# Performance work log

Measured on AMD Instinct MI355X. Metric: run time of the kernel, lower is better.

## Reference

```python
import jax, jax.numpy as jnp
import numpy as np
from jax import lax

T_LEN, BATCH, D_IN, D_HID, N_LAYERS = 512, 32, 512, 512, 4


def setup_inputs() -> dict:
    key = jax.random.key(0)
    kx, kw, ku = jax.random.split(key, 3)
    x = jax.random.normal(kx, (T_LEN, BATCH, D_IN), dtype=jnp.float32)
    # xavier-ish scale on input kernels to keep the relu recurrence stable
    W = jax.random.normal(kw, (N_LAYERS, D_HID, D_IN), dtype=jnp.float32) * (1.0 / np.sqrt(D_IN))
    b = jnp.zeros((N_LAYERS, D_HID), dtype=jnp.float32)
    # diagonal recurrent weights in [0,1) so |u|<=1 (non-exploding)
    u = jax.random.uniform(ku, (N_LAYERS, D_HID), dtype=jnp.float32)
    return {"x": x, "W": W, "b": b, "u": u}


def _indrnn_layer(x, W_l, b_l, u_l):
    # x: [T, B, Din]; precompute input projection as one big GEMM
    xh = jnp.einsum('tbd,hd->tbh', x, W_l) + b_l  # [T, B, Dh]
    h0 = jnp.zeros((x.shape[1], W_l.shape[0]), dtype=x.dtype)

    def step(h, xh_t):
        h_new = jax.nn.relu(xh_t + u_l * h)
        return h_new, h_new

    _, outs = lax.scan(step, h0, xh)
    return outs  # [T, B, Dh]


def reference(x, W, b, u):
    out = x
    for l in range(W.shape[0]):  # fixed small layer count
        out = _indrnn_layer(out, W[l], b[l], u[l])
    return out
```

## Files before the change

### kernel.cpp

```cpp
#include <hip/hip_runtime.h>
#include <hip/hip_bf16.h>

typedef short bf16x8 __attribute__((ext_vector_type(8)));
typedef float f32x4 __attribute__((ext_vector_type(4)));

#define T_LEN 512
#define BATCH 32
#define D 512
#define M_TOT (T_LEN * BATCH)
#define NLAYER 4

#define BM 128
#define BN 128
#define BK 64
#define NT (D / BK)
#define EP 72

#define CH 64
#define NCH (T_LEN / CH)

__global__ __launch_bounds__(256) void convert_k(const float* __restrict__ W,
                                                 const float* __restrict__ x,
                                                 __hip_bfloat16* __restrict__ Wb,
                                                 __hip_bfloat16* __restrict__ xb) {
    const int nW = NLAYER * D * D;
    const int nX = M_TOT * D;
    int i = (blockIdx.x * 256 + threadIdx.x) * 4;
    const float* src;
    __hip_bfloat16* dst;
    if (i < nW) {
        src = W + i;
        dst = Wb + i;
    } else {
        int k = i - nW;
        if (k >= nX) return;
        src = x + k;
        dst = xb + k;
    }
    float4 v = *(const float4*)src;
    __hip_bfloat16 h0 = __float2bfloat16(v.x);
    __hip_bfloat16 h1 = __float2bfloat16(v.y);
    __hip_bfloat16 h2 = __float2bfloat16(v.z);
    __hip_bfloat16 h3 = __float2bfloat16(v.w);
    ushort4 o;
    o.x = *(const unsigned short*)&h0;
    o.y = *(const unsigned short*)&h1;
    o.z = *(const unsigned short*)&h2;
    o.w = *(const unsigned short*)&h3;
    *(ushort4*)dst = o;
}

__global__ __launch_bounds__(256) void gemm_bt(const __hip_bfloat16* __restrict__ A,
                                               const __hip_bfloat16* __restrict__ Bt,
                                               const float* __restrict__ bias,
                                               __hip_bfloat16* __restrict__ Cb) {
    constexpr int K = D;
    constexpr int N = D;
    __shared__ __hip_bfloat16 smem[4 * BM * BK];
    __hip_bfloat16* const AsP[2] = {smem, smem + BM * BK};
    __hip_bfloat16* const BsP[2] = {smem + 2 * BM * BK, smem + 3 * BM * BK};

    const int tid  = threadIdx.x;
    const int wave = tid >> 6;
    const int lane = tid & 63;

    const int bid = blockIdx.x;
    const int xcd = bid & 7;
    const int j   = bid >> 3;
    const int bm  = xcd * 16 + (j >> 2);
    const int bn  = j & 3;

    const int wm = (wave >> 1) * 64;
    const int wn = (wave & 1) * 64;

    const int srow = lane >> 3;
    const int scol = ((lane & 7) ^ srow) * 8;

    const __hip_bfloat16* Ag = A  + (size_t)(bm * BM) * K;
    const __hip_bfloat16* Bg = Bt + (size_t)(bn * BN) * K;

    f32x4 acc[4][4] = {};

#define STAGE(buf, k0)                                                                               \
    do {                                                                                             \
        _Pragma("unroll") for (int jj = 0; jj < 4; ++jj) {                                           \
            const int rbase = (jj * 4 + wave) * 8;                                                   \
            __builtin_amdgcn_global_load_lds(                                                        \
                (const __attribute__((address_space(1))) void*)(Ag + (size_t)(rbase + srow) * K + (k0) + scol), \
                (__attribute__((address_space(3))) void*)(&AsP[buf][rbase * BK]), 16, 0, 0);         \
            __builtin_amdgcn_global_load_lds(                                                        \
                (const __attribute__((address_space(1))) void*)(Bg + (size_t)(rbase + srow) * K + (k0) + scol), \
                (__attribute__((address_space(3))) void*)(&BsP[buf][rbase * BK]), 16, 0, 0);         \
        }                                                                                            \
    } while (0)

#define COMPUTE(buf)                                                                                 \
    do {                                                                                             \
        bf16x8 af[4][2], bv[4][2];                                                                   \
        const int fr = lane & 15;                                                                    \
        const int kq = lane >> 4;                                                          \
        _Pragma("unroll") for (int mi = 0; mi < 4; ++mi) {                                           \
            const int r = wm + mi * 16 + fr;                                                         \
            _Pragma("unroll") for (int kh = 0; kh < 2; ++kh) {                                       \
                const int c = ((kh * 4 + kq) ^ (fr & 7)) * 8;                                        \
                af[mi][kh] = *(const bf16x8*)(&AsP[buf][r * BK + c]);                                \
            }                                                                                        \
        }                                                                                            \
        _Pragma("unroll") for (int ni = 0; ni < 4; ++ni) {                                           \
            const int r = wn + ni * 16 + fr;                                                         \
            _Pragma("unroll") for (int kh = 0; kh < 2; ++kh) {                                       \
                const int c = ((kh * 4 + kq) ^ (fr & 7)) * 8;                                        \
                bv[ni][kh] = *(const bf16x8*)(&BsP[buf][r * BK + c]);                                \
            }                                                                                        \
        }                                                                                            \
        _Pragma("unroll") for (int kh = 0; kh < 2; ++kh)                                             \
            _Pragma("unroll") for (int mi = 0; mi < 4; ++mi)                                         \
                _Pragma("unroll") for (int ni = 0; ni < 4; ++ni)                                     \
                    acc[mi][ni] = __builtin_amdgcn_mfma_f32_16x16x32_bf16(af[mi][kh], bv[ni][kh],    \
                                                                          acc[mi][ni], 0, 0, 0);    \
    } while (0)

    STAGE(0, 0);
    __syncthreads();
    int cur = 0;
#pragma unroll
    for (int kt = 1; kt < NT; ++kt) {
        STAGE(cur ^ 1, kt * BK);
        COMPUTE(cur);
        __syncthreads();
        cur ^= 1;
    }
    COMPUTE(cur);
    __syncthreads();

    {
        __hip_bfloat16* S = smem + wave * (64 * EP);
        const int cfr = lane & 15;
        const int cfq = lane >> 4;
        float bs[4];
#pragma unroll
        for (int ni = 0; ni < 4; ++ni) bs[ni] = bias[bn * BN + wn + ni * 16 + cfr];
#pragma unroll
        for (int mi = 0; mi < 4; ++mi)
#pragma unroll
            for (int ni = 0; ni < 4; ++ni)
#pragma unroll
                for (int r = 0; r < 4; ++r)
                    S[(mi * 16 + cfq * 4 + r) * EP + ni * 16 + cfr] =
                        __float2bfloat16(acc[mi][ni][r] + bs[ni]);
        const int rq = lane >> 3;
        const int cl = (lane & 7) * 8;
#pragma unroll
        for (int p = 0; p < 8; ++p) {
            const int lr = p * 8 + rq;
            bf16x8 v = *(const bf16x8*)(S + lr * EP + cl);
            *(bf16x8*)(&Cb[(size_t)(bm * BM + wm + lr) * N + bn * BN + wn + cl]) = v;
        }
    }
#undef STAGE
#undef COMPUTE
}

template <int MODE>
__global__ __launch_bounds__(512) void scan_k(const __hip_bfloat16* __restrict__ xh,
                                              const float* __restrict__ u,
                                              float* __restrict__ outf,
                                              __hip_bfloat16* __restrict__ outb) {
    __shared__ float2 md[NCH][64];
    const int i   = threadIdx.x & 63;
    const int c   = threadIdx.x >> 6;
    const int idx = blockIdx.x * 64 + i;
    const float uu = u[idx & (D - 1)];

    const __hip_bfloat16* p = xh + (size_t)c * CH * M_TOT + idx;
    unsigned short xv[CH];
#pragma unroll
    for (int t = 0; t < CH; ++t) xv[t] = *(const unsigned short*)(p + (size_t)t * M_TOT);

    float m = 0.f, d = 0.f;
#pragma unroll
    for (int t = 0; t < CH; ++t) {
        const float a = __uint_as_float(((unsigned int)xv[t]) << 16);
        m = fmaxf(fmaf(uu, m, a), 0.f);
        d = fmaf(uu, d, a);
    }
    md[c][i] = make_float2(m, d);
    __syncthreads();

    float e = uu * uu;
    e *= e; e *= e; e *= e; e *= e; e *= e;
    float h = 0.f;
    for (int jj = 0; jj < c; ++jj) {
        const float2 v = md[jj][i];
        h = fmaxf(v.x, fmaf(e, h, v.y));
    }

    float* qf = outf + (size_t)c * CH * M_TOT + idx;
    __hip_bfloat16* qb = outb + (size_t)c * CH * M_TOT + idx;
#pragma unroll
    for (int t = 0; t < CH; ++t) {
        const float a = __uint_as_float(((unsigned int)xv[t]) << 16);
        h = fmaxf(fmaf(uu, h, a), 0.f);
        if (MODE & 1) qf[(size_t)t * M_TOT] = h;
        if (MODE & 2) qb[(size_t)t * M_TOT] = __float2bfloat16(h);
    }
}

extern "C" void kernel_launch(void* const* d_in, const int* in_sizes, int n_in,
                              void* d_out, int out_size, void* d_ws, size_t ws_size,
                              hipStream_t stream) {
    const float* x = (const float*)d_in[0];
    const float* W = (const float*)d_in[1];
    const float* b = (const float*)d_in[2];
    const float* u = (const float*)d_in[3];
    float* out = (float*)d_out;

    __hip_bfloat16* Wb = (__hip_bfloat16*)d_ws;
    __hip_bfloat16* Ab = (__hip_bfloat16*)((char*)d_ws + (size_t)NLAYER * D * D * 2);
    __hip_bfloat16* Xh = Ab + (size_t)M_TOT * D;

    const int n_conv = NLAYER * D * D + M_TOT * D;
    convert_k<<<n_conv / 4 / 256, 256, 0, stream>>>(W, x, Wb, Ab);

    for (int l = 0; l < NLAYER; ++l) {
        gemm_bt<<<(M_TOT / BM) * (D / BN), 256, 0, stream>>>(Ab, Wb + (size_t)l * D * D,
                                                             b + (size_t)l * D, Xh);
        if (l < NLAYER - 1) {
            scan_k<2><<<M_TOT / 64, 512, 0, stream>>>(Xh, u + (size_t)l * D, nullptr, Ab);
        } else {
            scan_k<1><<<M_TOT / 64, 512, 0, stream>>>(Xh, u + (size_t)l * D, out, nullptr);
        }
    }
}
```

Measured before the change: 124.9 us.

## Fuse input fp32-to-bf16 conversion into first GEMM and halve scan chunk length

The standalone conversion of x to bf16 is removed. The first-layer GEMM now loads fp32 A tiles into registers, converts them, and writes them to LDS in the existing swizzled layout, saving a full read/write pass over the activations. The scan kernel now uses 32-step chunks, with each thread handling two adjacent hidden units through packed 32-bit loads and stores. This shortens the serial recurrence per chunk at the cost of a longer carry-combine loop. The fp32 A path loses the async global-to-LDS loads, so the first GEMM has to hide register-staged load latency behind compute.

```diff
diff --git a/kernel.cpp b/kernel.cpp
--- a/kernel.cpp
+++ b/kernel.cpp
@@ -16,28 +16,13 @@
 #define NT (D / BK)
 #define EP 72
 
-#define CH 64
+#define CH 32
 #define NCH (T_LEN / CH)
 
 __global__ __launch_bounds__(256) void convert_k(const float* __restrict__ W,
-                                                 const float* __restrict__ x,
-                                                 __hip_bfloat16* __restrict__ Wb,
-                                                 __hip_bfloat16* __restrict__ xb) {
-    const int nW = NLAYER * D * D;
-    const int nX = M_TOT * D;
-    int i = (blockIdx.x * 256 + threadIdx.x) * 4;
-    const float* src;
-    __hip_bfloat16* dst;
-    if (i < nW) {
-        src = W + i;
-        dst = Wb + i;
-    } else {
-        int k = i - nW;
-        if (k >= nX) return;
-        src = x + k;
-        dst = xb + k;
-    }
-    float4 v = *(const float4*)src;
+                                                 __hip_bfloat16* __restrict__ Wb) {
+    const int i = (blockIdx.x * 256 + threadIdx.x) * 4;
+    float4 v = *(const float4*)(W + i);
     __hip_bfloat16 h0 = __float2bfloat16(v.x);
     __hip_bfloat16 h1 = __float2bfloat16(v.y);
     __hip_bfloat16 h2 = __float2bfloat16(v.z);
@@ -47,10 +32,11 @@
     o.y = *(const unsigned short*)&h1;
     o.z = *(const unsigned short*)&h2;
     o.w = *(const unsigned short*)&h3;
-    *(ushort4*)dst = o;
-}
-
-__global__ __launch_bounds__(256) void gemm_bt(const __hip_bfloat16* __restrict__ A,
+    *(ushort4*)(Wb + i) = o;
+}
+
+template <bool AF32>
+__global__ __launch_bounds__(256) void gemm_bt(const void* __restrict__ Avp,
                                                const __hip_bfloat16* __restrict__ Bt,
                                                const float* __restrict__ bias,
                                                __hip_bfloat16* __restrict__ Cb) {
@@ -66,9 +52,9 @@
 
     const int bid = blockIdx.x;
     const int xcd = bid & 7;
-    const int j   = bid >> 3;
-    const int bm  = xcd * 16 + (j >> 2);
-    const int bn  = j & 3;
+    const int jb  = bid >> 3;
+    const int bm  = xcd * 16 + (jb >> 2);
+    const int bn  = jb & 3;
 
     const int wm = (wave >> 1) * 64;
     const int wn = (wave & 1) * 64;
@@ -76,29 +62,64 @@
     const int srow = lane >> 3;
     const int scol = ((lane & 7) ^ srow) * 8;
 
-    const __hip_bfloat16* Ag = A  + (size_t)(bm * BM) * K;
+    const __hip_bfloat16* Ag = AF32 ? nullptr
+                                    : (const __hip_bfloat16*)Avp + (size_t)(bm * BM) * K;
+    const float* Agf = AF32 ? (const float*)Avp + (size_t)(bm * BM) * K : nullptr;
     const __hip_bfloat16* Bg = Bt + (size_t)(bn * BN) * K;
 
     f32x4 acc[4][4] = {};
-
-#define STAGE(buf, k0)                                                                               \
+    float4 va[4][2];
+
+#define STAGE_A_LDS(buf, k0)                                                                         \
     do {                                                                                             \
         _Pragma("unroll") for (int jj = 0; jj < 4; ++jj) {                                           \
             const int rbase = (jj * 4 + wave) * 8;                                                   \
             __builtin_amdgcn_global_load_lds(                                                        \
                 (const __attribute__((address_space(1))) void*)(Ag + (size_t)(rbase + srow) * K + (k0) + scol), \
                 (__attribute__((address_space(3))) void*)(&AsP[buf][rbase * BK]), 16, 0, 0);         \
+        }                                                                                            \
+    } while (0)
+
+#define STAGE_B(buf, k0)                                                                             \
+    do {                                                                                             \
+        _Pragma("unroll") for (int jj = 0; jj < 4; ++jj) {                                           \
+            const int rbase = (jj * 4 + wave) * 8;                                                   \
             __builtin_amdgcn_global_load_lds(                                                        \
                 (const __attribute__((address_space(1))) void*)(Bg + (size_t)(rbase + srow) * K + (k0) + scol), \
                 (__attribute__((address_space(3))) void*)(&BsP[buf][rbase * BK]), 16, 0, 0);         \
         }                                                                                            \
     } while (0)
 
+#define LOAD_A_F32(k0)                                                                               \
+    do {                                                                                             \
+        _Pragma("unroll") for (int jj = 0; jj < 4; ++jj) {                                           \
+            const int rbase = (jj * 4 + wave) * 8;                                                   \
+            const float* s = Agf + (size_t)(rbase + srow) * K + (k0) + scol;                         \
+            va[jj][0] = *(const float4*)s;                                                           \
+            va[jj][1] = *(const float4*)(s + 4);                                                     \
+        }                                                                                            \
+    } while (0)
+
+#define WRITE_A_F32(buf)                                                                             \
+    do {                                                                                             \
+        _Pragma("unroll") for (int jj = 0; jj < 4; ++jj) {                                           \
+            const int rbase = (jj * 4 + wave) * 8;                                                   \
+            bf16x8 pk;                                                                               \
+            _Pragma("unroll") for (int q = 0; q < 4; ++q) {                                          \
+                __hip_bfloat16 t0 = __float2bfloat16(((const float*)&va[jj][0])[q]);                 \
+                __hip_bfloat16 t1 = __float2bfloat16(((const float*)&va[jj][1])[q]);                 \
+                pk[q]     = *(const short*)&t0;                                                      \
+                pk[q + 4] = *(const short*)&t1;                                                      \
+            }                                                                                        \
+            *(bf16x8*)(&AsP[buf][(rbase + srow) * BK + (lane & 7) * 8]) = pk;                        \
+        }                                                                                            \
+    } while (0)
+
 #define COMPUTE(buf)                                                                                 \
     do {                                                                                             \
         bf16x8 af[4][2], bv[4][2];                                                                   \
         const int fr = lane & 15;                                                                    \
-        const int kq = lane >> 4;                                                          \
+        const int kq = lane >> 4;                                                                    \
         _Pragma("unroll") for (int mi = 0; mi < 4; ++mi) {                                           \
             const int r = wm + mi * 16 + fr;                                                         \
             _Pragma("unroll") for (int kh = 0; kh < 2; ++kh) {                                       \
@@ -120,17 +141,37 @@
                                                                           acc[mi][ni], 0, 0, 0);    \
     } while (0)
 
-    STAGE(0, 0);
-    __syncthreads();
-    int cur = 0;
-#pragma unroll
-    for (int kt = 1; kt < NT; ++kt) {
-        STAGE(cur ^ 1, kt * BK);
+    if constexpr (AF32) {
+        LOAD_A_F32(0);
+        STAGE_B(0, 0);
+        WRITE_A_F32(0);
+        __syncthreads();
+        int cur = 0;
+#pragma unroll
+        for (int kt = 1; kt < NT; ++kt) {
+            LOAD_A_F32(kt * BK);
+            STAGE_B(cur ^ 1, kt * BK);
+            COMPUTE(cur);
+            WRITE_A_F32(cur ^ 1);
+            __syncthreads();
+            cur ^= 1;
+        }
         COMPUTE(cur);
+    } else {
+        STAGE_A_LDS(0, 0);
+        STAGE_B(0, 0);
         __syncthreads();
-        cur ^= 1;
-    }
-    COMPUTE(cur);
+        int cur = 0;
+#pragma unroll
+        for (int kt = 1; kt < NT; ++kt) {
+            STAGE_A_LDS(cur ^ 1, kt * BK);
+            STAGE_B(cur ^ 1, kt * BK);
+            COMPUTE(cur);
+            __syncthreads();
+            cur ^= 1;
+        }
+        COMPUTE(cur);
+    }
     __syncthreads();
 
     {
@@ -157,7 +198,10 @@
             *(bf16x8*)(&Cb[(size_t)(bm * BM + wm + lr) * N + bn * BN + wn + cl]) = v;
         }
     }
-#undef STAGE
+#undef STAGE_A_LDS
+#undef STAGE_B
+#undef LOAD_A_F32
+#undef WRITE_A_F32
 #undef COMPUTE
 }
 
@@ -166,43 +210,57 @@
                                               const float* __restrict__ u,
                                               float* __restrict__ outf,
                                               __hip_bfloat16* __restrict__ outb) {
-    __shared__ float2 md[NCH][64];
-    const int i   = threadIdx.x & 63;
-    const int c   = threadIdx.x >> 6;
-    const int idx = blockIdx.x * 64 + i;
-    const float uu = u[idx & (D - 1)];
+    __shared__ float4 md[NCH][32];
+    const int i2  = threadIdx.x & 31;
+    const int c   = threadIdx.x >> 5;
+    const int idx = blockIdx.x * 64 + i2 * 2;
+    const float u0 = u[idx & (D - 1)];
+    const float u1 = u[(idx + 1) & (D - 1)];
 
     const __hip_bfloat16* p = xh + (size_t)c * CH * M_TOT + idx;
-    unsigned short xv[CH];
-#pragma unroll
-    for (int t = 0; t < CH; ++t) xv[t] = *(const unsigned short*)(p + (size_t)t * M_TOT);
-
-    float m = 0.f, d = 0.f;
+    unsigned int xv[CH];
+#pragma unroll
+    for (int t = 0; t < CH; ++t) xv[t] = *(const unsigned int*)(p + (size_t)t * M_TOT);
+
+    float m0 = 0.f, d0 = 0.f, m1 = 0.f, d1 = 0.f;
 #pragma unroll
     for (int t = 0; t < CH; ++t) {
-        const float a = __uint_as_float(((unsigned int)xv[t]) << 16);
-        m = fmaxf(fmaf(uu, m, a), 0.f);
-        d = fmaf(uu, d, a);
-    }
-    md[c][i] = make_float2(m, d);
+        const float a0 = __uint_as_float(xv[t] << 16);
+        const float a1 = __uint_as_float(xv[t] & 0xffff0000u);
+        m0 = fmaxf(fmaf(u0, m0, a0), 0.f);
+        d0 = fmaf(u0, d0, a0);
+        m1 = fmaxf(fmaf(u1, m1, a1), 0.f);
+        d1 = fmaf(u1, d1, a1);
+    }
+    md[c][i2] = make_float4(m0, d0, m1, d1);
     __syncthreads();
 
-    float e = uu * uu;
-    e *= e; e *= e; e *= e; e *= e; e *= e;
-    float h = 0.f;
+    float e0 = u0 * u0, e1 = u1 * u1;
+    e0 *= e0; e0 *= e0; e0 *= e0; e0 *= e0;
+    e1 *= e1; e1 *= e1; e1 *= e1; e1 *= e1;
+    float h0 = 0.f, h1 = 0.f;
     for (int jj = 0; jj < c; ++jj) {
-        const float2 v = md[jj][i];
-        h = fmaxf(v.x, fmaf(e, h, v.y));
-    }
-
-    float* qf = outf + (size_t)c * CH * M_TOT + idx;
-    __hip_bfloat16* qb = outb + (size_t)c * CH * M_TOT + idx;
+        const float4 v = md[jj][i2];
+        h0 = fmaxf(v.x, fmaf(e0, h0, v.y));
+        h1 = fmaxf(v.z, fmaf(e1, h1, v.w));
+    }
+
+    const size_t base = (size_t)c * CH * M_TOT + idx;
 #pragma unroll
     for (int t = 0; t < CH; ++t) {
-        const float a = __uint_as_float(((unsigned int)xv[t]) << 16);
-        h = fmaxf(fmaf(uu, h, a), 0.f);
-        if (MODE & 1) qf[(size_t)t * M_TOT] = h;
-        if (MODE & 2) qb[(size_t)t * M_TOT] = __float2bfloat16(h);
+        const size_t off = base + (size_t)t * M_TOT;
+        const float a0 = __uint_as_float(xv[t] << 16);
+        const float a1 = __uint_as_float(xv[t] & 0xffff0000u);
+        h0 = fmaxf(fmaf(u0, h0, a0), 0.f);
+        h1 = fmaxf(fmaf(u1, h1, a1), 0.f);
+        if (MODE & 1) *(float2*)(outf + off) = make_float2(h0, h1);
+        if (MODE & 2) {
+            __hip_bfloat16 b0 = __float2bfloat16(h0);
+            __hip_bfloat16 b1 = __float2bfloat16(h1);
+            unsigned int pk = (unsigned int)(*(unsigned short*)&b0) |
+                              ((unsigned int)(*(unsigned short*)&b1) << 16);
+            *(unsigned int*)(outb + off) = pk;
+        }
     }
 }
 
@@ -219,12 +277,16 @@
     __hip_bfloat16* Ab = (__hip_bfloat16*)((char*)d_ws + (size_t)NLAYER * D * D * 2);
     __hip_bfloat16* Xh = Ab + (size_t)M_TOT * D;
 
-    const int n_conv = NLAYER * D * D + M_TOT * D;
-    convert_k<<<n_conv / 4 / 256, 256, 0, stream>>>(W, x, Wb, Ab);
+    convert_k<<<(NLAYER * D * D / 4) / 256, 256, 0, stream>>>(W, Wb);
 
     for (int l = 0; l < NLAYER; ++l) {
-        gemm_bt<<<(M_TOT / BM) * (D / BN), 256, 0, stream>>>(Ab, Wb + (size_t)l * D * D,
-                                                             b + (size_t)l * D, Xh);
+        if (l == 0) {
+            gemm_bt<true><<<(M_TOT / BM) * (D / BN), 256, 0, stream>>>(
+                (const void*)x, Wb, b, Xh);
+        } else {
+            gemm_bt<false><<<(M_TOT / BM) * (D / BN), 256, 0, stream>>>(
+                (const void*)Ab, Wb + (size_t)l * D * D, b + (size_t)l * D, Xh);
+        }
         if (l < NLAYER - 1) {
             scan_k<2><<<M_TOT / 64, 512, 0, stream>>>(Xh, u + (size_t)l * D, nullptr, Ab);
         } else {
```

Result: faster. 116.3 us (-6.9%).
